# Kernel tuning notes

Hardware: AMD Instinct MI355X
Metric: run time of the kernel (lower is better)

The kernel has to match this reference:

```python
import jax, jax.numpy as jnp
import numpy as np

B, N, E, H = 2, 2048, 1024, 16
D = E // H  # head_dim = 64


def setup_inputs() -> dict:
    key = jax.random.key(0)
    ks = jax.random.split(key, 8)
    s = 1.0 / np.sqrt(D)
    return {
        "query": jax.random.normal(ks[0], (B, N, E), jnp.float32),
        "key": jax.random.normal(ks[1], (B, N, E), jnp.float32),
        "value": jax.random.normal(ks[2], (B, N, E), jnp.float32),
        "mask": jax.random.randint(ks[3], (B, N), 0, 2, jnp.int32),
        # per-head Linear weights, torch layout (out_features, in_features) stacked over heads
        "Wq": jax.random.uniform(ks[4], (H, D, D), jnp.float32, -s, s),
        "Wk": jax.random.uniform(ks[5], (H, D, D), jnp.float32, -s, s),
        "Wv": jax.random.uniform(ks[6], (H, D, D), jnp.float32, -s, s),
        "Wo": jax.random.uniform(ks[7], (E, E), jnp.float32, -1.0 / np.sqrt(E), 1.0 / np.sqrt(E)),
    }


def reference(query, key, value, mask, Wq, Wk, Wv, Wo):
    b, n, e = query.shape
    h, d, _ = Wq.shape
    q = query.reshape(b, n, h, d)
    k = key.reshape(b, n, h, d)
    v = value.reshape(b, n, h, d)
    # per-head Linear (no bias): x @ W[i].T, batched over heads
    qh = jnp.einsum('bnhd,hed->bnhe', q, Wq)
    kh = jnp.einsum('bnhd,hed->bnhe', k, Wk)
    vh = jnp.einsum('bnhd,hed->bnhe', v, Wv)
    # NOTE: original scales by sqrt(embed_size), not sqrt(head_dim)
    scores = jnp.einsum('bqhd,bkhd->bhqk', qh, kh) / (e ** 0.5)
    # NOTE: mask is unsqueezed on the KEY axis position in torch (dim=2),
    # so it masks entire QUERY rows, broadcasting over keys.
    scores = jnp.where(mask[:, None, :, None] == 0, jnp.float32(-1e28), scores)
    probs = jax.nn.softmax(scores, axis=-1)
    attn = jnp.einsum('bhqk,bkhd->bqhd', probs, vh).reshape(b, n, e)
    return attn @ Wo.T
```

## Files before the change

kernel.cpp:

```cpp
#include <hip/hip_runtime.h>
#include <hip/hip_bf16.h>

#define B_ 2
#define N_ 2048
#define E_ 1024
#define H_ 16
#define D_ 64
#define BH_ (B_ * H_)

typedef __attribute__((ext_vector_type(4))) float f32x4;
typedef __attribute__((ext_vector_type(8))) short bf16x8;
typedef __attribute__((ext_vector_type(4))) short s16x4;
typedef __attribute__((ext_vector_type(4))) int i32x4;

#define MFMA(a, b, c) __builtin_amdgcn_mfma_f32_16x16x32_bf16(a, b, c, 0, 0, 0)

#define AS1(p) ((const __attribute__((address_space(1))) unsigned int*)(p))
#define AS3(p) ((__attribute__((address_space(3))) unsigned int*)(p))

static __device__ __forceinline__ unsigned short f2bf(float f) {
    unsigned int u = __builtin_bit_cast(unsigned int, f);
    u += 0x7fff + ((u >> 16) & 1);
    return (unsigned short)(u >> 16);
}
static __device__ __forceinline__ float bf2f(unsigned short s) {
    unsigned int u = ((unsigned int)s) << 16;
    return __builtin_bit_cast(float, u);
}
static __device__ __forceinline__ int pack2bf(float lo, float hi) {
    return (int)f2bf(lo) | ((int)f2bf(hi) << 16);
}
static __device__ __forceinline__ bf16x8 cvt8s(const float* __restrict__ p, float sc) {
    f32x4 a = *(const f32x4*)p;
    f32x4 b = *(const f32x4*)(p + 4);
    bf16x8 r;
    r[0] = (short)f2bf(a.x * sc); r[1] = (short)f2bf(a.y * sc);
    r[2] = (short)f2bf(a.z * sc); r[3] = (short)f2bf(a.w * sc);
    r[4] = (short)f2bf(b.x * sc); r[5] = (short)f2bf(b.y * sc);
    r[6] = (short)f2bf(b.z * sc); r[7] = (short)f2bf(b.w * sc);
    return r;
}

__global__ __launch_bounds__(256, 4)
void proj_kernel(const float* __restrict__ q, const float* __restrict__ k,
                 const float* __restrict__ v,
                 const float* __restrict__ Wq, const float* __restrict__ Wk,
                 const float* __restrict__ Wv,
                 const int* __restrict__ mask,
                 unsigned short* __restrict__ qh, unsigned short* __restrict__ kh,
                 unsigned short* __restrict__ vt) {
    const int z = blockIdx.z;
    const float* X = (z == 0) ? q : (z == 1) ? k : v;
    const float* W = (z == 0) ? Wq : (z == 1) ? Wk : Wv;
    unsigned short* out = (z == 0) ? qh : (z == 1) ? kh : vt;
    const float wscale = (z == 0) ? (1.44269504f * 0.03125f) : 1.0f;

    const int lane = threadIdx.x & 63;
    const int wave = threadIdx.x >> 6;
    const int l16  = lane & 15;
    const int quad = lane >> 4;
    const int bh = blockIdx.y;
    const int b = bh >> 4, h = bh & 15;
    const int n0 = blockIdx.x * 64;
    const int tok = n0 + wave * 16 + l16;

    const float* xrow = X + ((size_t)(b * N_ + tok)) * E_ + h * 64;
    bf16x8 xf[2];
    xf[0] = cvt8s(xrow + quad * 8, 1.0f);
    xf[1] = cvt8s(xrow + 32 + quad * 8, 1.0f);

    const float* Wh = W + (size_t)h * 64 * 64;
    bf16x8 wf[4][2];
#pragma unroll
    for (int t4 = 0; t4 < 4; ++t4) {
        const float* wrow = Wh + (t4 * 16 + l16) * 64;
        wf[t4][0] = cvt8s(wrow + quad * 8, wscale);
        wf[t4][1] = cvt8s(wrow + 32 + quad * 8, wscale);
    }

    const int mk = (z == 0) ? mask[b * N_ + tok] : 1;

#pragma unroll
    for (int mi = 0; mi < 4; ++mi) {
        f32x4 a = {0.f, 0.f, 0.f, 0.f};
        a = MFMA(wf[mi][0], xf[0], a);
        a = MFMA(wf[mi][1], xf[1], a);
        if (z != 2) {
            s16x4 pk = {(short)f2bf(a.x), (short)f2bf(a.y),
                        (short)f2bf(a.z), (short)f2bf(a.w)};
            if (!mk) pk = (s16x4){0, 0, 0, 0};
            *(s16x4*)(out + ((size_t)bh * N_ + tok) * 64 + mi * 16 + quad * 4) = pk;
        } else {
#pragma unroll
            for (int r = 0; r < 4; ++r) {
                int dout = mi * 16 + quad * 4 + r;
                out[((size_t)bh * 64 + dout) * N_ + tok] = (unsigned short)f2bf(a[r]);
            }
        }
    }
}

__global__ __launch_bounds__(256)
void cvt_wo_kernel(const float* __restrict__ wo, unsigned short* __restrict__ wob) {
    int idx = blockIdx.x * 256 + threadIdx.x;
    f32x4 v = *(const f32x4*)(wo + (size_t)idx * 4);
    s16x4 r = {(short)f2bf(v.x), (short)f2bf(v.y), (short)f2bf(v.z), (short)f2bf(v.w)};
    *(s16x4*)(wob + (size_t)idx * 4) = r;
}

__global__ __launch_bounds__(256, 2)
void attn_kernel(const unsigned short* __restrict__ qh,
                 const unsigned short* __restrict__ kh,
                 const unsigned short* __restrict__ vt,
                 unsigned short* __restrict__ attnb) {
    __shared__ short Kb[2][4096];
    __shared__ short Vb[2][4096];

    const int tid  = threadIdx.x;
    const int lane = tid & 63;
    const int wave = tid >> 6;
    const int l16  = lane & 15;
    const int quad = lane >> 4;

    const int flat = blockIdx.y * gridDim.x + blockIdx.x;
    const int qblk = flat >> 5;
    const int rem  = flat & 31;
    const int bh   = ((rem & 7) << 2) | (rem >> 3);
    const int b = bh >> 4, h = bh & 15;
    const int q0 = qblk * 128 + wave * 32;

    const unsigned short* kbase = kh + (size_t)bh * N_ * 64;
    const unsigned short* vbase = vt + (size_t)bh * 64 * N_;

    const int c0i = tid;
    const int c1i = tid + 256;
    const int l0 = ((c0i & 7) * 64 + (c0i >> 3)) * 8;
    const int l1 = ((c1i & 7) * 64 + (c1i >> 3)) * 8;

    const int srcA = (((quad * 2) & 3) << 4) + l16;
    const int srcB = (((quad * 2 + 1) & 3) << 4) + l16;
    const bool hiSel = (quad >= 2);

    bf16x8 qf[2][2];
#pragma unroll
    for (int qi = 0; qi < 2; ++qi) {
        const unsigned short* qrow = qh + ((size_t)bh * N_ + q0 + qi * 16 + l16) * 64;
        qf[qi][0] = *(const bf16x8*)(qrow + quad * 8);
        qf[qi][1] = *(const bf16x8*)(qrow + 32 + quad * 8);
    }

    float lI[2] = {0.f, 0.f};
    f32x4 o[4][2];
#pragma unroll
    for (int mi = 0; mi < 4; ++mi)
#pragma unroll
        for (int qi = 0; qi < 2; ++qi) o[mi][qi] = (f32x4){0.f, 0.f, 0.f, 0.f};

    bf16x8 gK0, gK1, gV0, gV1;
    gK0 = *(const bf16x8*)(kbase + c0i * 8);
    gK1 = *(const bf16x8*)(kbase + c1i * 8);
    gV0 = *(const bf16x8*)(vbase + (size_t)(c0i >> 3) * N_ + (c0i & 7) * 8);
    gV1 = *(const bf16x8*)(vbase + (size_t)(c1i >> 3) * N_ + (c1i & 7) * 8);
    *(bf16x8*)(&Kb[0][l0]) = gK0;
    *(bf16x8*)(&Kb[0][l1]) = gK1;
    *(bf16x8*)(&Vb[0][l0]) = gV0;
    *(bf16x8*)(&Vb[0][l1]) = gV1;
    __syncthreads();

    for (int kt = 0; kt < N_ / 64; ++kt) {
        const int cur = kt & 1;

        if (kt + 1 < N_ / 64) {
            const int k0n = (kt + 1) * 64;
            gK0 = *(const bf16x8*)(kbase + (size_t)k0n * 64 + c0i * 8);
            gK1 = *(const bf16x8*)(kbase + (size_t)k0n * 64 + c1i * 8);
            gV0 = *(const bf16x8*)(vbase + (size_t)(c0i >> 3) * N_ + k0n + (c0i & 7) * 8);
            gV1 = *(const bf16x8*)(vbase + (size_t)(c1i >> 3) * N_ + k0n + (c1i & 7) * 8);
        }

        bf16x8 ka[4][2];
#pragma unroll
        for (int t4 = 0; t4 < 4; ++t4) {
            ka[t4][0] = *(const bf16x8*)(&Kb[cur][(quad * 64 + t4 * 16 + l16) * 8]);
            ka[t4][1] = *(const bf16x8*)(&Kb[cur][((4 + quad) * 64 + t4 * 16 + l16) * 8]);
        }

        f32x4 s[2][4];
#pragma unroll
        for (int qi = 0; qi < 2; ++qi)
#pragma unroll
            for (int t4 = 0; t4 < 4; ++t4) {
                f32x4 z = {0.f, 0.f, 0.f, 0.f};
                z = MFMA(ka[t4][0], qf[qi][0], z);
                z = MFMA(ka[t4][1], qf[qi][1], z);
                s[qi][t4] = z;
            }

        bf16x8 va[4][2];
#pragma unroll
        for (int mi = 0; mi < 4; ++mi) {
            va[mi][0] = *(const bf16x8*)(&Vb[cur][(quad * 64 + mi * 16 + l16) * 8]);
            va[mi][1] = *(const bf16x8*)(&Vb[cur][((4 + quad) * 64 + mi * 16 + l16) * 8]);
        }

#pragma unroll
        for (int qi = 0; qi < 2; ++qi) {
            float rsum = 0.f;
            int pk[4][2];
#pragma unroll
            for (int t4 = 0; t4 < 4; ++t4) {
                f32x4 p;
#pragma unroll
                for (int r = 0; r < 4; ++r) {
                    p[r] = __builtin_amdgcn_exp2f(s[qi][t4][r]);
                    rsum += p[r];
                }
                pk[t4][0] = pack2bf(p.x, p.y);
                pk[t4][1] = pack2bf(p.z, p.w);
            }
            rsum += __shfl_xor(rsum, 16);
            rsum += __shfl_xor(rsum, 32);
            lI[qi] += rsum;

            i32x4 w0, w1;
#pragma unroll
            for (int d = 0; d < 2; ++d) {
                int a0 = __shfl(pk[0][d], srcA), a1 = __shfl(pk[1][d], srcA);
                int b0 = __shfl(pk[0][d], srcB), b1 = __shfl(pk[1][d], srcB);
                w0[d]     = hiSel ? a1 : a0;
                w0[2 + d] = hiSel ? b1 : b0;
                int c0 = __shfl(pk[2][d], srcA), c1 = __shfl(pk[3][d], srcA);
                int e0 = __shfl(pk[2][d], srcB), e1 = __shfl(pk[3][d], srcB);
                w1[d]     = hiSel ? c1 : c0;
                w1[2 + d] = hiSel ? e1 : e0;
            }
            bf16x8 pb0 = __builtin_bit_cast(bf16x8, w0);
            bf16x8 pb1 = __builtin_bit_cast(bf16x8, w1);

#pragma unroll
            for (int mi = 0; mi < 4; ++mi) {
                o[mi][qi] = MFMA(va[mi][0], pb0, o[mi][qi]);
                o[mi][qi] = MFMA(va[mi][1], pb1, o[mi][qi]);
            }
        }

        if (kt + 1 < N_ / 64) {
            const int nxt = cur ^ 1;
            *(bf16x8*)(&Kb[nxt][l0]) = gK0;
            *(bf16x8*)(&Kb[nxt][l1]) = gK1;
            *(bf16x8*)(&Vb[nxt][l0]) = gV0;
            *(bf16x8*)(&Vb[nxt][l1]) = gV1;
            __syncthreads();
        }
    }

#pragma unroll
    for (int qi = 0; qi < 2; ++qi) {
        const float inv = 1.0f / lI[qi];
        const int qrow_idx = q0 + qi * 16 + l16;
#pragma unroll
        for (int mi = 0; mi < 4; ++mi) {
            f32x4 ov = o[mi][qi];
            s16x4 pkk = {(short)f2bf(ov.x * inv), (short)f2bf(ov.y * inv),
                         (short)f2bf(ov.z * inv), (short)f2bf(ov.w * inv)};
            int d0 = mi * 16 + quad * 4;
            *(s16x4*)(attnb + ((size_t)(b * N_ + qrow_idx)) * E_ + h * 64 + d0) = pkk;
        }
    }
}

__global__ __launch_bounds__(512, 1)
void out_gemm_kernel(const unsigned short* __restrict__ A,
                     const unsigned short* __restrict__ Bw,
                     float* __restrict__ out) {
    __shared__ short As[2][128 * 32];
    __shared__ short Bs[2][128 * 32];

    const int tid  = threadIdx.x;
    const int lane = tid & 63;
    const int l16  = lane & 15;
    const int quad = lane >> 4;
    const int wave = tid >> 6;
    const int wm = wave & 1, wn = wave >> 1;
    const int m0 = blockIdx.x * 128;
    const int n0 = blockIdx.y * 128;

    const unsigned short* gA = A + (size_t)m0 * E_;
    const unsigned short* gB = Bw + (size_t)n0 * E_;

    f32x4 acc[4][2];
#pragma unroll
    for (int mt = 0; mt < 4; ++mt)
#pragma unroll
        for (int nt = 0; nt < 2; ++nt) acc[mt][nt] = (f32x4){0.f, 0.f, 0.f, 0.f};

    const int cc = tid >> 7, rr = tid & 127;
#define OG_STAGE(buf, k0)                                                        \
    {                                                                            \
        __builtin_amdgcn_global_load_lds(AS1(gA + (size_t)rr * E_ + (k0) + cc * 8), \
                                         AS3(&As[buf][tid * 8]), 16, 0, 0);      \
        __builtin_amdgcn_global_load_lds(AS1(gB + (size_t)rr * E_ + (k0) + cc * 8), \
                                         AS3(&Bs[buf][tid * 8]), 16, 0, 0);      \
    }

    OG_STAGE(0, 0)
    __syncthreads();

    for (int kt = 0; kt < E_ / 32; ++kt) {
        const int cur = kt & 1;
        if (kt + 1 < E_ / 32) OG_STAGE(cur ^ 1, (kt + 1) * 32)

        bf16x8 af[4], bf[2];
#pragma unroll
        for (int mt = 0; mt < 4; ++mt)
            af[mt] = *(const bf16x8*)(&As[cur][(quad * 128 + wm * 64 + mt * 16 + l16) * 8]);
#pragma unroll
        for (int nt = 0; nt < 2; ++nt)
            bf[nt] = *(const bf16x8*)(&Bs[cur][(quad * 128 + wn * 32 + nt * 16 + l16) * 8]);

#pragma unroll
        for (int mt = 0; mt < 4; ++mt)
#pragma unroll
            for (int nt = 0; nt < 2; ++nt)
                acc[mt][nt] = MFMA(af[mt], bf[nt], acc[mt][nt]);

        __syncthreads();
    }

#pragma unroll
    for (int mt = 0; mt < 4; ++mt)
#pragma unroll
        for (int nt = 0; nt < 2; ++nt)
#pragma unroll
            for (int r = 0; r < 4; ++r)
                out[(size_t)(m0 + wm * 64 + mt * 16 + quad * 4 + r) * E_ +
                    n0 + wn * 32 + nt * 16 + l16] = acc[mt][nt][r];
#undef OG_STAGE
}

extern "C" void kernel_launch(void* const* d_in, const int* in_sizes, int n_in,
                              void* d_out, int out_size, void* d_ws, size_t ws_size,
                              hipStream_t stream) {
    const float* q    = (const float*)d_in[0];
    const float* k    = (const float*)d_in[1];
    const float* v    = (const float*)d_in[2];
    const int*   mask = (const int*)d_in[3];
    const float* Wq   = (const float*)d_in[4];
    const float* Wk   = (const float*)d_in[5];
    const float* Wv   = (const float*)d_in[6];
    const float* Wo   = (const float*)d_in[7];
    float* out = (float*)d_out;

    char* ws = (char*)d_ws;
    unsigned short* qh    = (unsigned short*)(ws);
    unsigned short* kh    = (unsigned short*)(ws + (size_t)8 * 1024 * 1024);
    unsigned short* vt    = (unsigned short*)(ws + (size_t)16 * 1024 * 1024);
    unsigned short* attnb = (unsigned short*)(ws + (size_t)24 * 1024 * 1024);
    unsigned short* wob   = (unsigned short*)(ws);

    dim3 blk(256);
    proj_kernel<<<dim3(N_ / 64, BH_, 3), blk, 0, stream>>>(q, k, v, Wq, Wk, Wv, mask,
                                                           qh, kh, vt);
    attn_kernel<<<dim3(16, 32), blk, 0, stream>>>(qh, kh, vt, attnb);
    cvt_wo_kernel<<<dim3(E_ * E_ / 1024), blk, 0, stream>>>(Wo, wob);
    out_gemm_kernel<<<dim3(32, 8), dim3(512), 0, stream>>>(attnb, wob, out);
}
```

Before: 237.1 us.

## Software-pipeline PV MFMAs one tile behind, pad LDS rows, use packed bf16 converts

The attention loop now runs the P·V MFMAs for the previous key tile while the current tile's QK and exp work proceeds. This needs a third V buffer in LDS, and the last tile's P·V is done in an epilogue. The change is meant to hide exp and shuffle latency behind matrix work. K and V shared tiles switch from a swizzled layout to a row-major layout padded to 72 shorts per row, to avoid bank conflicts. Scalar float-to-bf16 rounding is replaced with the packed __float22bfloat162_rn intrinsic across all kernels. The extra V buffer raises LDS use, and the carried pb registers raise register pressure.

```diff
diff --git a/kernel.cpp b/kernel.cpp
--- a/kernel.cpp
+++ b/kernel.cpp
@@ -12,6 +12,7 @@
 typedef __attribute__((ext_vector_type(8))) short bf16x8;
 typedef __attribute__((ext_vector_type(4))) short s16x4;
 typedef __attribute__((ext_vector_type(4))) int i32x4;
+typedef __attribute__((ext_vector_type(2))) int i32x2;
 
 #define MFMA(a, b, c) __builtin_amdgcn_mfma_f32_16x16x32_bf16(a, b, c, 0, 0, 0)
 
@@ -23,22 +24,18 @@
     u += 0x7fff + ((u >> 16) & 1);
     return (unsigned short)(u >> 16);
 }
-static __device__ __forceinline__ float bf2f(unsigned short s) {
-    unsigned int u = ((unsigned int)s) << 16;
-    return __builtin_bit_cast(float, u);
-}
 static __device__ __forceinline__ int pack2bf(float lo, float hi) {
-    return (int)f2bf(lo) | ((int)f2bf(hi) << 16);
+    __hip_bfloat162 t = __float22bfloat162_rn(float2{lo, hi});
+    int r;
+    __builtin_memcpy(&r, &t, 4);
+    return r;
 }
 static __device__ __forceinline__ bf16x8 cvt8s(const float* __restrict__ p, float sc) {
     f32x4 a = *(const f32x4*)p;
     f32x4 b = *(const f32x4*)(p + 4);
-    bf16x8 r;
-    r[0] = (short)f2bf(a.x * sc); r[1] = (short)f2bf(a.y * sc);
-    r[2] = (short)f2bf(a.z * sc); r[3] = (short)f2bf(a.w * sc);
-    r[4] = (short)f2bf(b.x * sc); r[5] = (short)f2bf(b.y * sc);
-    r[6] = (short)f2bf(b.z * sc); r[7] = (short)f2bf(b.w * sc);
-    return r;
+    i32x4 r = {pack2bf(a.x * sc, a.y * sc), pack2bf(a.z * sc, a.w * sc),
+               pack2bf(b.x * sc, b.y * sc), pack2bf(b.z * sc, b.w * sc)};
+    return __builtin_bit_cast(bf16x8, r);
 }
 
 __global__ __launch_bounds__(256, 4)
@@ -86,10 +83,9 @@
         a = MFMA(wf[mi][0], xf[0], a);
         a = MFMA(wf[mi][1], xf[1], a);
         if (z != 2) {
-            s16x4 pk = {(short)f2bf(a.x), (short)f2bf(a.y),
-                        (short)f2bf(a.z), (short)f2bf(a.w)};
-            if (!mk) pk = (s16x4){0, 0, 0, 0};
-            *(s16x4*)(out + ((size_t)bh * N_ + tok) * 64 + mi * 16 + quad * 4) = pk;
+            i32x2 pk = {pack2bf(a.x, a.y), pack2bf(a.z, a.w)};
+            if (!mk) pk = (i32x2){0, 0};
+            *(i32x2*)(out + ((size_t)bh * N_ + tok) * 64 + mi * 16 + quad * 4) = pk;
         } else {
 #pragma unroll
             for (int r = 0; r < 4; ++r) {
@@ -104,8 +100,8 @@
 void cvt_wo_kernel(const float* __restrict__ wo, unsigned short* __restrict__ wob) {
     int idx = blockIdx.x * 256 + threadIdx.x;
     f32x4 v = *(const f32x4*)(wo + (size_t)idx * 4);
-    s16x4 r = {(short)f2bf(v.x), (short)f2bf(v.y), (short)f2bf(v.z), (short)f2bf(v.w)};
-    *(s16x4*)(wob + (size_t)idx * 4) = r;
+    i32x2 r = {pack2bf(v.x, v.y), pack2bf(v.z, v.w)};
+    *(i32x2*)(wob + (size_t)idx * 4) = r;
 }
 
 __global__ __launch_bounds__(256, 2)
@@ -113,8 +109,8 @@
                  const unsigned short* __restrict__ kh,
                  const unsigned short* __restrict__ vt,
                  unsigned short* __restrict__ attnb) {
-    __shared__ short Kb[2][4096];
-    __shared__ short Vb[2][4096];
+    __shared__ short Kb[2][64][72];
+    __shared__ short Vb[3][64][72];
 
     const int tid  = threadIdx.x;
     const int lane = tid & 63;
@@ -134,8 +130,14 @@
 
     const int c0i = tid;
     const int c1i = tid + 256;
-    const int l0 = ((c0i & 7) * 64 + (c0i >> 3)) * 8;
-    const int l1 = ((c1i & 7) * 64 + (c1i >> 3)) * 8;
+    const int o0 = (c0i >> 3) * 72 + (c0i & 7) * 8;
+    const int o1 = (c1i >> 3) * 72 + (c1i & 7) * 8;
+
+    short* kcur  = &Kb[0][0][0];
+    short* knext = &Kb[1][0][0];
+    short* vprev = &Vb[2][0][0];
+    short* vcur  = &Vb[0][0][0];
+    short* vnext = &Vb[1][0][0];
 
     const int srcA = (((quad * 2) & 3) << 4) + l16;
     const int srcB = (((quad * 2 + 1) & 3) << 4) + l16;
@@ -155,21 +157,21 @@
     for (int mi = 0; mi < 4; ++mi)
 #pragma unroll
         for (int qi = 0; qi < 2; ++qi) o[mi][qi] = (f32x4){0.f, 0.f, 0.f, 0.f};
+
+    bf16x8 pb[2][2];
 
     bf16x8 gK0, gK1, gV0, gV1;
     gK0 = *(const bf16x8*)(kbase + c0i * 8);
     gK1 = *(const bf16x8*)(kbase + c1i * 8);
     gV0 = *(const bf16x8*)(vbase + (size_t)(c0i >> 3) * N_ + (c0i & 7) * 8);
     gV1 = *(const bf16x8*)(vbase + (size_t)(c1i >> 3) * N_ + (c1i & 7) * 8);
-    *(bf16x8*)(&Kb[0][l0]) = gK0;
-    *(bf16x8*)(&Kb[0][l1]) = gK1;
-    *(bf16x8*)(&Vb[0][l0]) = gV0;
-    *(bf16x8*)(&Vb[0][l1]) = gV1;
+    *(bf16x8*)(kcur + o0) = gK0;
+    *(bf16x8*)(kcur + o1) = gK1;
+    *(bf16x8*)(vcur + o0) = gV0;
+    *(bf16x8*)(vcur + o1) = gV1;
     __syncthreads();
 
     for (int kt = 0; kt < N_ / 64; ++kt) {
-        const int cur = kt & 1;
-
         if (kt + 1 < N_ / 64) {
             const int k0n = (kt + 1) * 64;
             gK0 = *(const bf16x8*)(kbase + (size_t)k0n * 64 + c0i * 8);
@@ -181,8 +183,8 @@
         bf16x8 ka[4][2];
 #pragma unroll
         for (int t4 = 0; t4 < 4; ++t4) {
-            ka[t4][0] = *(const bf16x8*)(&Kb[cur][(quad * 64 + t4 * 16 + l16) * 8]);
-            ka[t4][1] = *(const bf16x8*)(&Kb[cur][((4 + quad) * 64 + t4 * 16 + l16) * 8]);
+            ka[t4][0] = *(const bf16x8*)(kcur + (t4 * 16 + l16) * 72 + quad * 8);
+            ka[t4][1] = *(const bf16x8*)(kcur + (t4 * 16 + l16) * 72 + 32 + quad * 8);
         }
 
         f32x4 s[2][4];
@@ -196,11 +198,20 @@
                 s[qi][t4] = z;
             }
 
-        bf16x8 va[4][2];
-#pragma unroll
-        for (int mi = 0; mi < 4; ++mi) {
-            va[mi][0] = *(const bf16x8*)(&Vb[cur][(quad * 64 + mi * 16 + l16) * 8]);
-            va[mi][1] = *(const bf16x8*)(&Vb[cur][((4 + quad) * 64 + mi * 16 + l16) * 8]);
+        if (kt > 0) {
+            bf16x8 va[4][2];
+#pragma unroll
+            for (int mi = 0; mi < 4; ++mi) {
+                va[mi][0] = *(const bf16x8*)(vprev + (mi * 16 + l16) * 72 + quad * 8);
+                va[mi][1] = *(const bf16x8*)(vprev + (mi * 16 + l16) * 72 + 32 + quad * 8);
+            }
+#pragma unroll
+            for (int mi = 0; mi < 4; ++mi)
+#pragma unroll
+                for (int qi = 0; qi < 2; ++qi) {
+                    o[mi][qi] = MFMA(va[mi][0], pb[qi][0], o[mi][qi]);
+                    o[mi][qi] = MFMA(va[mi][1], pb[qi][1], o[mi][qi]);
+                }
         }
 
 #pragma unroll
@@ -234,24 +245,36 @@
                 w1[d]     = hiSel ? c1 : c0;
                 w1[2 + d] = hiSel ? e1 : e0;
             }
-            bf16x8 pb0 = __builtin_bit_cast(bf16x8, w0);
-            bf16x8 pb1 = __builtin_bit_cast(bf16x8, w1);
-
-#pragma unroll
-            for (int mi = 0; mi < 4; ++mi) {
-                o[mi][qi] = MFMA(va[mi][0], pb0, o[mi][qi]);
-                o[mi][qi] = MFMA(va[mi][1], pb1, o[mi][qi]);
-            }
+            pb[qi][0] = __builtin_bit_cast(bf16x8, w0);
+            pb[qi][1] = __builtin_bit_cast(bf16x8, w1);
         }
 
         if (kt + 1 < N_ / 64) {
-            const int nxt = cur ^ 1;
-            *(bf16x8*)(&Kb[nxt][l0]) = gK0;
-            *(bf16x8*)(&Kb[nxt][l1]) = gK1;
-            *(bf16x8*)(&Vb[nxt][l0]) = gV0;
-            *(bf16x8*)(&Vb[nxt][l1]) = gV1;
+            *(bf16x8*)(knext + o0) = gK0;
+            *(bf16x8*)(knext + o1) = gK1;
+            *(bf16x8*)(vnext + o0) = gV0;
+            *(bf16x8*)(vnext + o1) = gV1;
             __syncthreads();
         }
+
+        short* t = kcur; kcur = knext; knext = t;
+        short* tv = vprev; vprev = vcur; vcur = vnext; vnext = tv;
+    }
+
+    {
+        bf16x8 va[4][2];
+#pragma unroll
+        for (int mi = 0; mi < 4; ++mi) {
+            va[mi][0] = *(const bf16x8*)(vprev + (mi * 16 + l16) * 72 + quad * 8);
+            va[mi][1] = *(const bf16x8*)(vprev + (mi * 16 + l16) * 72 + 32 + quad * 8);
+        }
+#pragma unroll
+        for (int mi = 0; mi < 4; ++mi)
+#pragma unroll
+            for (int qi = 0; qi < 2; ++qi) {
+                o[mi][qi] = MFMA(va[mi][0], pb[qi][0], o[mi][qi]);
+                o[mi][qi] = MFMA(va[mi][1], pb[qi][1], o[mi][qi]);
+            }
     }
 
 #pragma unroll
@@ -261,10 +284,10 @@
 #pragma unroll
         for (int mi = 0; mi < 4; ++mi) {
             f32x4 ov = o[mi][qi];
-            s16x4 pkk = {(short)f2bf(ov.x * inv), (short)f2bf(ov.y * inv),
-                         (short)f2bf(ov.z * inv), (short)f2bf(ov.w * inv)};
+            i32x2 pkk = {pack2bf(ov.x * inv, ov.y * inv),
+                         pack2bf(ov.z * inv, ov.w * inv)};
             int d0 = mi * 16 + quad * 4;
-            *(s16x4*)(attnb + ((size_t)(b * N_ + qrow_idx)) * E_ + h * 64 + d0) = pkk;
+            *(i32x2*)(attnb + ((size_t)(b * N_ + qrow_idx)) * E_ + h * 64 + d0) = pkk;
         }
     }
 }
```

Result: faster. 222.3 us (-6.3%).
